# Kernel tuning notes

Measured on AMD Instinct MI355X. Metric: run time of the kernel, lower is better.

The kernel has to match this reference:

```python
import jax, jax.numpy as jnp
import numpy as np

TARGET_FIDELITY = 0.95
WEIGHT = 0.1
BATCH, DIM = 8192, 2048


def setup_inputs() -> dict:
    key = jax.random.key(0)
    k1, k2 = jax.random.split(key)
    # Scale by 1/sqrt(DIM) so each row is roughly unit-norm (quantum-state-like)
    # and the trace fidelity lands strictly inside the clamp interval [0, 1].
    scale = 1.0 / np.sqrt(DIM)
    latent_codes = jax.random.normal(k1, (BATCH, DIM), dtype=jnp.float32) * scale
    target_codes = jax.random.normal(k2, (BATCH, DIM), dtype=jnp.float32) * scale
    return {"latent_codes": latent_codes, "target_codes": target_codes}


def reference(latent_codes, target_codes):
    batch = latent_codes.shape[0]
    # rho = mean_i z_i z_i^T  ==  L^T L / B  (single GEMM instead of B outer products)
    rho = jnp.matmul(latent_codes.T, latent_codes) / batch      # [D, D]
    sigma = jnp.matmul(target_codes.T, target_codes) / batch    # [D, D]
    # trace(rho @ sigma) = sum(rho * sigma) since both are symmetric
    fidelity = jnp.clip(jnp.sum(rho * sigma), 0.0, 1.0)
    loss = WEIGHT * jnp.abs(fidelity - TARGET_FIDELITY)
    return loss
```

## Files before the change

### kernel.cpp

```cpp
#include <hip/hip_runtime.h>
#include <stdint.h>

#define BATCH 8192
#define DIM   2048
#define NT    272
#define QTOT  (NT * 32)
#define QPB   17
#define NSLOT 768
#define DOTBLK (136 * 16)

typedef unsigned char  u8;
typedef unsigned short u16;
typedef unsigned int   u32;

using v8i   = __attribute__((ext_vector_type(8)))  int;
using v16f  = __attribute__((ext_vector_type(16))) float;

#if __has_builtin(__builtin_amdgcn_cvt_scalef32_pk_fp4_f32)
#define HW_FP4 1
#endif

__device__ __forceinline__ void gl_lds16(const void* g, void* l) {
  __builtin_amdgcn_global_load_lds(
      (const __attribute__((address_space(1))) u32*)g,
      (__attribute__((address_space(3))) u32*)l, 16, 0, 0);
}

__device__ __forceinline__ int piece_base(int b) {
  const int m = b & 31;
  const int p = (m <= 16) ? (m >> 1) : (8 + ((m - 15) >> 1));
  return b + 16 * (b >> 5) + p;
}

__device__ __forceinline__ u32 bfpair(float x, float y) {
  u32 bx = __float_as_uint(x);
  u32 by = __float_as_uint(y);
  bx = (bx + 0x7FFFu + ((bx >> 16) & 1u)) >> 16;
  by = (by + 0x7FFFu + ((by >> 16) & 1u)) >> 16;
  return bx | (by << 16);
}
__device__ __forceinline__ float bflo(u32 w) { return __uint_as_float(w << 16); }
__device__ __forceinline__ float bfhi(u32 w) { return __uint_as_float(w & 0xFFFF0000u); }

__device__ __forceinline__ u32 nib4(float x) {
  float xs = x * 64.0f;
  float a  = fabsf(xs);
  u32 n = (u32)(a >= 0.25f) + (u32)(a >= 0.75f) + (u32)(a >= 1.25f) +
          (u32)(a >= 1.75f) + (u32)(a >= 2.5f)  + (u32)(a >= 3.5f)  +
          (u32)(a >= 5.0f);
  return n | (xs < 0.0f ? 8u : 0u);
}

__device__ __forceinline__ u16 pack4_fp4(float a, float b, float c, float d) {
#ifdef HW_FP4
  u32 w = __builtin_amdgcn_cvt_scalef32_pk_fp4_f32(0u,  a * 64.0f, b * 64.0f, 1.0f, 0);
  w     = __builtin_amdgcn_cvt_scalef32_pk_fp4_f32(w,   c * 64.0f, d * 64.0f, 1.0f, 1);
  return (u16)w;
#else
  return (u16)(nib4(a) | (nib4(b) << 4) | (nib4(c) << 8) | (nib4(d) << 12));
#endif
}

__global__ __launch_bounds__(256) void tcvt_fp4(
    const float* __restrict__ L, const float* __restrict__ T,
    u8* __restrict__ X, u8* __restrict__ Y)
{
  __shared__ u16 ls[64 * 68];

  const int tid = threadIdx.x;

  int id = blockIdx.x;
  const float* src;
  u8* dst;
  if (id < 1024) { src = L; dst = X; }
  else           { src = T; dst = Y; id -= 1024; }
  const int d0 = (id & 31) * 64;
  const int b0 = (id >> 5) * 256;

  const int s  = tid & 15;
  const int g  = tid >> 4;
  const int sw = s & 12;

  float4 f[4][4];
#pragma unroll
  for (int j = 0; j < 4; ++j)
#pragma unroll
    for (int r = 0; r < 4; ++r)
      f[j][r] = *(const float4*)(src + (size_t)(b0 + j * 64 + g * 4 + r) * DIM
                                 + d0 + s * 4);

#pragma unroll
  for (int j = 0; j < 4; ++j) {
    const int w = (j * 16 + g) ^ sw;
    const float* fp[4] = {(const float*)&f[j][0], (const float*)&f[j][1],
                          (const float*)&f[j][2], (const float*)&f[j][3]};
#pragma unroll
    for (int i = 0; i < 4; ++i)
      ls[(s * 4 + i) * 68 + w] = pack4_fp4(fp[0][i], fp[1][i], fp[2][i], fp[3][i]);
  }
  __syncthreads();

#pragma unroll
  for (int j2 = 0; j2 < 2; ++j2) {
    const int d   = (tid >> 3) + j2 * 32;
    const int o8  = tid & 7;
    const int gsw = (d >> 4) & 3;
    const int g1  = (2 * o8)     ^ gsw;
    const int g2  = (2 * o8 + 1) ^ gsw;
    uint2 a = *(const uint2*)&ls[d * 68 + g1 * 4];
    uint2 b = *(const uint2*)&ls[d * 68 + g2 * 4];
    uint4 v = {a.x, a.y, b.x, b.y};
    *(uint4*)(dst + (size_t)(d0 + d) * (BATCH / 2) + (b0 >> 1) + o8 * 16) = v;
  }
}

__global__ __launch_bounds__(256, 2) void gram_fp4(
    const u8* __restrict__ X, const u8* __restrict__ Y,
    u32* __restrict__ P)
{
  __shared__ u8 ls[2][2][16384];

  const int tid = threadIdx.x;
  const int bid = blockIdx.x;

  const int wave = tid >> 6;
  const int lane = tid & 63;
  const int wr = (wave >> 1) * 64;
  const int wc = (wave & 1) * 64;
  const int lr = lane & 31;
  const int kh = lane >> 5;

  u32 sdst[4]; int srow[4], sgc16[4];
#pragma unroll
  for (int rr = 0; rr < 4; ++rr) {
    const int li  = rr * 256 + tid;
    const int row = li >> 3;
    const int p   = li & 7;
    sdst[rr]  = (u32)(row * 128 + p * 16);
    srow[rr]  = row;
    sgc16[rr] = (p ^ (row & 7)) * 16;
  }

  u32 fa[2][4], fb[2][4];
#pragma unroll
  for (int h = 0; h < 2; ++h) {
    const int ra = wr + h * 32 + lr;
    const int rb = wc + h * 32 + lr;
#pragma unroll
    for (int ks = 0; ks < 4; ++ks) {
      const int c = 2 * ks + kh;
      fa[h][ks] = (u32)(ra * 128 + (c ^ (ra & 7)) * 16);
      fb[h][ks] = (u32)(rb * 128 + (c ^ (rb & 7)) * 16);
    }
  }

  v16f acc[2][2] = {};
  const int sc = 0x7F7F7F7F;

  const int q0  = bid * QPB;
  const int t0b = q0 >> 5;
  const int sl0 = piece_base(bid);
  int cur_t = -1, buf = 0;
  bool diag = false;
  const u8* src = X;
  u32 soi[4], soj[4];

  for (int it = 0; it < QPB; ++it) {
    const int q = q0 + it;
    const int t = q >> 5;
    const int k = q & 31;

    if (t != cur_t) {
      const int ltile = (t < 136) ? t : t - 136;
      src = (t < 136) ? X : Y;
      int ti = 0;
      while ((ti + 1) * (ti + 2) / 2 <= ltile) ++ti;
      const int tj = ltile - ti * (ti + 1) / 2;
      const int i0 = ti * 128;
      const int j0 = tj * 128;
      diag = (ti == tj);
#pragma unroll
      for (int rr = 0; rr < 4; ++rr) {
        soi[rr] = (u32)(i0 + srow[rr]) * (BATCH / 2) + sgc16[rr];
        soj[rr] = (u32)(j0 + srow[rr]) * (BATCH / 2) + sgc16[rr];
      }
      const u32 kb = (u32)k * 128;
#pragma unroll
      for (int rr = 0; rr < 4; ++rr)
        gl_lds16(src + soi[rr] + kb, &ls[buf][0][sdst[rr]]);
      if (!diag)
#pragma unroll
        for (int rr = 0; rr < 4; ++rr)
          gl_lds16(src + soj[rr] + kb, &ls[buf][1][sdst[rr]]);
      if (cur_t >= 0) {
        uint2* o = (uint2*)(P + (size_t)(sl0 + (cur_t - t0b)) * 8192);
#pragma unroll
        for (int h = 0; h < 2; ++h)
#pragma unroll
          for (int hc = 0; hc < 2; ++hc)
#pragma unroll
            for (int r4 = 0; r4 < 4; ++r4) {
              uint2 v = {bfpair(acc[h][hc][r4 * 4 + 0], acc[h][hc][r4 * 4 + 1]),
                         bfpair(acc[h][hc][r4 * 4 + 2], acc[h][hc][r4 * 4 + 3])};
              o[((h * 2 + hc) * 4 + r4) * 256 + tid] = v;
            }
#pragma unroll
        for (int h = 0; h < 2; ++h)
#pragma unroll
          for (int hc = 0; hc < 2; ++hc)
#pragma unroll
            for (int c2 = 0; c2 < 16; ++c2)
              acc[h][hc][c2] = 0.0f;
      }
      cur_t = t;
    }

    __syncthreads();
    if (it + 1 < QPB && ((q + 1) >> 5) == t) {
      const u32 kb = (u32)(k + 1) * 128;
#pragma unroll
      for (int rr = 0; rr < 4; ++rr)
        gl_lds16(src + soi[rr] + kb, &ls[buf ^ 1][0][sdst[rr]]);
      if (!diag)
#pragma unroll
        for (int rr = 0; rr < 4; ++rr)
          gl_lds16(src + soj[rr] + kb, &ls[buf ^ 1][1][sdst[rr]]);
    }

    const u8* pI = ls[buf][0];
    const u8* pJ = diag ? ls[buf][0] : ls[buf][1];
#pragma unroll
    for (int ks = 0; ks < 4; ++ks) {
      v8i a[2], b[2];
#pragma unroll
      for (int h = 0; h < 2; ++h) {
        int4 pa = *(const int4*)&pI[fa[h][ks]];
        a[h] = (v8i){pa.x, pa.y, pa.z, pa.w, 0, 0, 0, 0};
        int4 pb = *(const int4*)&pJ[fb[h][ks]];
        b[h] = (v8i){pb.x, pb.y, pb.z, pb.w, 0, 0, 0, 0};
      }
#pragma unroll
      for (int h = 0; h < 2; ++h)
#pragma unroll
        for (int hc = 0; hc < 2; ++hc)
          acc[h][hc] = __builtin_amdgcn_mfma_scale_f32_32x32x64_f8f6f4(
              a[h], b[hc], acc[h][hc],  4,  4,
              0, sc, 0, sc);
    }
    buf ^= 1;
  }

  {
    uint2* o = (uint2*)(P + (size_t)(sl0 + (cur_t - t0b)) * 8192);
#pragma unroll
    for (int h = 0; h < 2; ++h)
#pragma unroll
      for (int hc = 0; hc < 2; ++hc)
#pragma unroll
        for (int r4 = 0; r4 < 4; ++r4) {
          uint2 v = {bfpair(acc[h][hc][r4 * 4 + 0], acc[h][hc][r4 * 4 + 1]),
                     bfpair(acc[h][hc][r4 * 4 + 2], acc[h][hc][r4 * 4 + 3])};
          o[((h * 2 + hc) * 4 + r4) * 256 + tid] = v;
        }
  }
}

__device__ __forceinline__ int collect_pieces(int t, int* s) {
  const int qlo = 32 * t, qhi = 32 * t + 31;
  const int b_lo = qlo / 17, b_hi = qhi / 17;
  int n = 0;
  for (int b = b_lo; b <= b_hi; ++b) {
    const int tfirst = (17 * b) >> 5;
    s[n++] = piece_base(b) + (t - tfirst);
  }
  return n;
}

__global__ __launch_bounds__(256) void dot_kernel(
    const uint2* __restrict__ P2, float* __restrict__ pd)
{
  __shared__ float red[4];
  const int tid  = threadIdx.x;
  const int lane = tid & 63;
  const int lt   = blockIdx.x >> 4;
  const int ch   = blockIdx.x & 15;

  int ti = 0;
  while ((ti + 1) * (ti + 2) / 2 <= lt) ++ti;
  const int tj = lt - ti * (ti + 1) / 2;
  const float w = (ti == tj) ? 1.0f : 2.0f;

  int sx[3], sy[3];
  const int nx = collect_pieces(lt, sx);
  const int ny = collect_pieces(136 + lt, sy);

  const int e = ch * 256 + tid;
  float a0, a1, a2, a3, b0, b1, b2, b3;
  {
    uint2 u = P2[(size_t)sx[0] * 4096 + e];
    a0 = bflo(u.x); a1 = bfhi(u.x); a2 = bflo(u.y); a3 = bfhi(u.y);
    u = P2[(size_t)sx[1] * 4096 + e];
    a0 += bflo(u.x); a1 += bfhi(u.x); a2 += bflo(u.y); a3 += bfhi(u.y);
    if (nx == 3) {
      u = P2[(size_t)sx[2] * 4096 + e];
      a0 += bflo(u.x); a1 += bfhi(u.x); a2 += bflo(u.y); a3 += bfhi(u.y);
    }
  }
  {
    uint2 u = P2[(size_t)sy[0] * 4096 + e];
    b0 = bflo(u.x); b1 = bfhi(u.x); b2 = bflo(u.y); b3 = bfhi(u.y);
    u = P2[(size_t)sy[1] * 4096 + e];
    b0 += bflo(u.x); b1 += bfhi(u.x); b2 += bflo(u.y); b3 += bfhi(u.y);
    if (ny == 3) {
      u = P2[(size_t)sy[2] * 4096 + e];
      b0 += bflo(u.x); b1 += bfhi(u.x); b2 += bflo(u.y); b3 += bfhi(u.y);
    }
  }
  float s = (a0 * b0 + a1 * b1 + a2 * b2 + a3 * b3) * w;

#pragma unroll
  for (int off = 32; off > 0; off >>= 1)
    s += __shfl_down(s, off);
  if (lane == 0) red[tid >> 6] = s;
  __syncthreads();
  if (tid == 0)
    pd[blockIdx.x] = red[0] + red[1] + red[2] + red[3];
}

__global__ __launch_bounds__(256) void fin_kernel(
    const float* __restrict__ pd, float* __restrict__ out)
{
  __shared__ float red[4];
  const int tid  = threadIdx.x;
  const int lane = tid & 63;
  float s = 0.0f;
  for (int i = tid; i < DOTBLK; i += 256) s += pd[i];
#pragma unroll
  for (int off = 32; off > 0; off >>= 1)
    s += __shfl_down(s, off);
  if (lane == 0) red[tid >> 6] = s;
  __syncthreads();
  if (tid == 0) {
    float S = red[0] + red[1] + red[2] + red[3];
    float fid = S * 0x1.0p-50f;
    fid = fminf(fmaxf(fid, 0.0f), 1.0f);
    *out = 0.1f * fabsf(fid - 0.95f);
  }
}

extern "C" void kernel_launch(void* const* d_in, const int* in_sizes, int n_in,
                              void* d_out, int out_size, void* d_ws, size_t ws_size,
                              hipStream_t stream) {
  const float* L = (const float*)d_in[0];
  const float* T = (const float*)d_in[1];
  float* out = (float*)d_out;

  const size_t NF4 = (size_t)BATCH * DIM / 2;
  u8*    X   = (u8*)d_ws;
  u8*    Y   = (u8*)d_ws + NF4;
  u32*   P   = (u32*)((char*)d_ws + 2 * NF4);
  float* pd  = (float*)(P + (size_t)NSLOT * 8192);

  tcvt_fp4<<<2048, 256, 0, stream>>>(L, T, X, Y);
  gram_fp4<<<512, 256, 0, stream>>>(X, Y, P);
  dot_kernel<<<DOTBLK, 256, 0, stream>>>((const uint2*)P, pd);
  fin_kernel<<<1, 256, 0, stream>>>(pd, out);
}
```

Baseline: 193.8 us.

## Split each gram tile into four fixed K-chunks with one block per chunk

Replaces the flat 17-quantum-per-block work split (512 blocks whose slices straddle tile boundaries, with a piece-index lookup) with a regular split of 1088 blocks, each computing one 128x128 tile over 8 K-steps and writing its own partial slot. The LDS buffer is single-buffered to halve shared memory, and launch bounds rise to 4 blocks per CU for more occupancy. The dot kernel now sums four fixed partials per tile. This gives up the double-buffered prefetch overlap, adds a second barrier per step, and adds more partial-tile traffic through the dot stage.

Measured after the change: 188.0 us. 1.03x faster.

```diff
diff --git a/kernel.cpp b/kernel.cpp
--- a/kernel.cpp
+++ b/kernel.cpp
@@ -5,8 +5,8 @@
 #define DIM   2048
 #define NT    272
 #define QTOT  (NT * 32)
-#define QPB   17
-#define NSLOT 768
+#define GQPB  8
+#define GBLK  (QTOT / GQPB)
 #define DOTBLK (136 * 16)
 
 typedef unsigned char  u8;
@@ -24,12 +24,6 @@
   __builtin_amdgcn_global_load_lds(
       (const __attribute__((address_space(1))) u32*)g,
       (__attribute__((address_space(3))) u32*)l, 16, 0, 0);
-}
-
-__device__ __forceinline__ int piece_base(int b) {
-  const int m = b & 31;
-  const int p = (m <= 16) ? (m >> 1) : (8 + ((m - 15) >> 1));
-  return b + 16 * (b >> 5) + p;
 }
 
 __device__ __forceinline__ u32 bfpair(float x, float y) {
@@ -114,11 +108,11 @@
   }
 }
 
-__global__ __launch_bounds__(256, 2) void gram_fp4(
+__global__ __launch_bounds__(256, 4) void gram_fp4(
     const u8* __restrict__ X, const u8* __restrict__ Y,
     u32* __restrict__ P)
 {
-  __shared__ u8 ls[2][2][16384];
+  __shared__ u8 ls[2][16384];
 
   const int tid = threadIdx.x;
   const int bid = blockIdx.x;
@@ -154,81 +148,42 @@
     }
   }
 
+  const int t  = bid >> 2;
+  const int k0 = (bid & 3) * GQPB;
+  const int ltile = (t < 136) ? t : t - 136;
+  const u8* src = (t < 136) ? X : Y;
+  int ti = 0;
+  while ((ti + 1) * (ti + 2) / 2 <= ltile) ++ti;
+  const int tj = ltile - ti * (ti + 1) / 2;
+  const int i0 = ti * 128;
+  const int j0 = tj * 128;
+  const bool diag = (ti == tj);
+
+  u32 soi[4], soj[4];
+#pragma unroll
+  for (int rr = 0; rr < 4; ++rr) {
+    soi[rr] = (u32)(i0 + srow[rr]) * (BATCH / 2) + sgc16[rr];
+    soj[rr] = (u32)(j0 + srow[rr]) * (BATCH / 2) + sgc16[rr];
+  }
+
   v16f acc[2][2] = {};
   const int sc = 0x7F7F7F7F;
 
-  const int q0  = bid * QPB;
-  const int t0b = q0 >> 5;
-  const int sl0 = piece_base(bid);
-  int cur_t = -1, buf = 0;
-  bool diag = false;
-  const u8* src = X;
-  u32 soi[4], soj[4];
-
-  for (int it = 0; it < QPB; ++it) {
-    const int q = q0 + it;
-    const int t = q >> 5;
-    const int k = q & 31;
-
-    if (t != cur_t) {
-      const int ltile = (t < 136) ? t : t - 136;
-      src = (t < 136) ? X : Y;
-      int ti = 0;
-      while ((ti + 1) * (ti + 2) / 2 <= ltile) ++ti;
-      const int tj = ltile - ti * (ti + 1) / 2;
-      const int i0 = ti * 128;
-      const int j0 = tj * 128;
-      diag = (ti == tj);
-#pragma unroll
-      for (int rr = 0; rr < 4; ++rr) {
-        soi[rr] = (u32)(i0 + srow[rr]) * (BATCH / 2) + sgc16[rr];
-        soj[rr] = (u32)(j0 + srow[rr]) * (BATCH / 2) + sgc16[rr];
-      }
-      const u32 kb = (u32)k * 128;
+  {
+    const u32 kb = (u32)k0 * 128;
+#pragma unroll
+    for (int rr = 0; rr < 4; ++rr)
+      gl_lds16(src + soi[rr] + kb, &ls[0][sdst[rr]]);
+    if (!diag)
 #pragma unroll
       for (int rr = 0; rr < 4; ++rr)
-        gl_lds16(src + soi[rr] + kb, &ls[buf][0][sdst[rr]]);
-      if (!diag)
-#pragma unroll
-        for (int rr = 0; rr < 4; ++rr)
-          gl_lds16(src + soj[rr] + kb, &ls[buf][1][sdst[rr]]);
-      if (cur_t >= 0) {
-        uint2* o = (uint2*)(P + (size_t)(sl0 + (cur_t - t0b)) * 8192);
-#pragma unroll
-        for (int h = 0; h < 2; ++h)
-#pragma unroll
-          for (int hc = 0; hc < 2; ++hc)
-#pragma unroll
-            for (int r4 = 0; r4 < 4; ++r4) {
-              uint2 v = {bfpair(acc[h][hc][r4 * 4 + 0], acc[h][hc][r4 * 4 + 1]),
-                         bfpair(acc[h][hc][r4 * 4 + 2], acc[h][hc][r4 * 4 + 3])};
-              o[((h * 2 + hc) * 4 + r4) * 256 + tid] = v;
-            }
-#pragma unroll
-        for (int h = 0; h < 2; ++h)
-#pragma unroll
-          for (int hc = 0; hc < 2; ++hc)
-#pragma unroll
-            for (int c2 = 0; c2 < 16; ++c2)
-              acc[h][hc][c2] = 0.0f;
-      }
-      cur_t = t;
-    }
-
+        gl_lds16(src + soj[rr] + kb, &ls[1][sdst[rr]]);
+  }
+
+  for (int it = 0; it < GQPB; ++it) {
     __syncthreads();
-    if (it + 1 < QPB && ((q + 1) >> 5) == t) {
-      const u32 kb = (u32)(k + 1) * 128;
-#pragma unroll
-      for (int rr = 0; rr < 4; ++rr)
-        gl_lds16(src + soi[rr] + kb, &ls[buf ^ 1][0][sdst[rr]]);
-      if (!diag)
-#pragma unroll
-        for (int rr = 0; rr < 4; ++rr)
-          gl_lds16(src + soj[rr] + kb, &ls[buf ^ 1][1][sdst[rr]]);
-    }
-
-    const u8* pI = ls[buf][0];
-    const u8* pJ = diag ? ls[buf][0] : ls[buf][1];
+    const u8* pI = ls[0];
+    const u8* pJ = diag ? ls[0] : ls[1];
 #pragma unroll
     for (int ks = 0; ks < 4; ++ks) {
       v8i a[2], b[2];
@@ -247,11 +202,21 @@
               a[h], b[hc], acc[h][hc],  4,  4,
               0, sc, 0, sc);
     }
-    buf ^= 1;
+    if (it + 1 < GQPB) {
+      __syncthreads();
+      const u32 kb = (u32)(k0 + it + 1) * 128;
+#pragma unroll
+      for (int rr = 0; rr < 4; ++rr)
+        gl_lds16(src + soi[rr] + kb, &ls[0][sdst[rr]]);
+      if (!diag)
+#pragma unroll
+        for (int rr = 0; rr < 4; ++rr)
+          gl_lds16(src + soj[rr] + kb, &ls[1][sdst[rr]]);
+    }
   }
 
   {
-    uint2* o = (uint2*)(P + (size_t)(sl0 + (cur_t - t0b)) * 8192);
+    uint2* o = (uint2*)(P + (size_t)bid * 8192);
 #pragma unroll
     for (int h = 0; h < 2; ++h)
 #pragma unroll
@@ -263,17 +228,6 @@
           o[((h * 2 + hc) * 4 + r4) * 256 + tid] = v;
         }
   }
-}
-
-__device__ __forceinline__ int collect_pieces(int t, int* s) {
-  const int qlo = 32 * t, qhi = 32 * t + 31;
-  const int b_lo = qlo / 17, b_hi = qhi / 17;
-  int n = 0;
-  for (int b = b_lo; b <= b_hi; ++b) {
-    const int tfirst = (17 * b) >> 5;
-    s[n++] = piece_base(b) + (t - tfirst);
-  }
-  return n;
 }
 
 __global__ __launch_bounds__(256) void dot_kernel(
@@ -290,31 +244,21 @@
   const int tj = lt - ti * (ti + 1) / 2;
   const float w = (ti == tj) ? 1.0f : 2.0f;
 
-  int sx[3], sy[3];
-  const int nx = collect_pieces(lt, sx);
-  const int ny = collect_pieces(136 + lt, sy);
-
-  const int e = ch * 256 + tid;
-  float a0, a1, a2, a3, b0, b1, b2, b3;
-  {
-    uint2 u = P2[(size_t)sx[0] * 4096 + e];
-    a0 = bflo(u.x); a1 = bfhi(u.x); a2 = bflo(u.y); a3 = bfhi(u.y);
-    u = P2[(size_t)sx[1] * 4096 + e];
+  const int e   = ch * 256 + tid;
+  const size_t sxb = (size_t)(4 * lt) * 4096 + e;
+  const size_t syb = (size_t)(4 * (136 + lt)) * 4096 + e;
+
+  float a0 = 0.f, a1 = 0.f, a2 = 0.f, a3 = 0.f;
+  float b0 = 0.f, b1 = 0.f, b2 = 0.f, b3 = 0.f;
+#pragma unroll
+  for (int i = 0; i < 4; ++i) {
+    uint2 u = P2[sxb + (size_t)i * 4096];
     a0 += bflo(u.x); a1 += bfhi(u.x); a2 += bflo(u.y); a3 += bfhi(u.y);
-    if (nx == 3) {
-      u = P2[(size_t)sx[2] * 4096 + e];
-      a0 += bflo(u.x); a1 += bfhi(u.x); a2 += bflo(u.y); a3 += bfhi(u.y);
-    }
-  }
-  {
-    uint2 u = P2[(size_t)sy[0] * 4096 + e];
-    b0 = bflo(u.x); b1 = bfhi(u.x); b2 = bflo(u.y); b3 = bfhi(u.y);
-    u = P2[(size_t)sy[1] * 4096 + e];
+  }
+#pragma unroll
+  for (int i = 0; i < 4; ++i) {
+    uint2 u = P2[syb + (size_t)i * 4096];
     b0 += bflo(u.x); b1 += bfhi(u.x); b2 += bflo(u.y); b3 += bfhi(u.y);
-    if (ny == 3) {
-      u = P2[(size_t)sy[2] * 4096 + e];
-      b0 += bflo(u.x); b1 += bfhi(u.x); b2 += bflo(u.y); b3 += bfhi(u.y);
-    }
   }
   float s = (a0 * b0 + a1 * b1 + a2 * b2 + a3 * b3) * w;
 
@@ -359,10 +303,10 @@
   u8*    X   = (u8*)d_ws;
   u8*    Y   = (u8*)d_ws + NF4;
   u32*   P   = (u32*)((char*)d_ws + 2 * NF4);
-  float* pd  = (float*)(P + (size_t)NSLOT * 8192);
+  float* pd  = (float*)(P + (size_t)GBLK * 8192);
 
   tcvt_fp4<<<2048, 256, 0, stream>>>(L, T, X, Y);
-  gram_fp4<<<512, 256, 0, stream>>>(X, Y, P);
+  gram_fp4<<<GBLK, 256, 0, stream>>>(X, Y, P);
   dot_kernel<<<DOTBLK, 256, 0, stream>>>((const uint2*)P, pd);
   fin_kernel<<<1, 256, 0, stream>>>(pd, out);
 }
```
